# Kernel tuning notes

Measured on AMD Instinct MI355X. Metric: run time of the kernel, lower is better.

The kernel has to match this reference:

```python
import jax, jax.numpy as jnp
import numpy as np

NUM_CLASSES = 21
EPS = 1e-6


def setup_inputs() -> dict:
    key = jax.random.key(0)
    k1, k2, k3 = jax.random.split(key, 3)
    feats = jax.random.normal(k1, (8, 256, 64, 64), dtype=jnp.float32)
    preds = jax.random.normal(k2, (8, NUM_CLASSES, 256, 256), dtype=jnp.float32)
    # labels in [0, 22): includes nclass=21 which acts as an ignore label
    masks = jax.random.randint(k3, (8, 256, 256), 0, 22, dtype=jnp.int64)
    return {"feats": feats, "preds": preds, "masks": masks}


def reference(feats, preds, masks):
    B, C = feats.shape[0], feats.shape[1]
    H, W = masks.shape[-2:]
    K = NUM_CLASSES

    # argmax over class logits -> predicted label map [B, H, W]
    pred_lbl = jnp.argmax(preds, axis=1)

    # bilinear upsample (align_corners=False, matches half-pixel resize)
    feats_up = jax.image.resize(feats, (B, C, H, W), method="bilinear")

    cls = jnp.arange(K)
    # one-hot of gt mask and of predictions; labels >= K (incl. 255) fall in
    # the dropped last channel of one_hot_2d, i.e. match no class here.
    gt_oh = (masks[:, None, :, :] == cls[None, :, None, None])      # [B,K,H,W]
    pr_oh = (pred_lbl[:, None, :, :] == cls[None, :, None, None])   # [B,K,H,W]
    joint = (gt_oh & pr_oh).astype(feats_up.dtype)                  # [B,K,H,W]

    counts = joint.sum(axis=(2, 3))                                  # [B,K]
    sums = jnp.einsum("bchw,bkhw->bkc", feats_up, joint)            # [B,K,C]

    # per-image class means (absent classes -> 0/eps = 0), then batch mean
    proto = (sums / (counts[..., None] + EPS)).mean(axis=0)          # [K,C]
    return proto
```

## Files before the change

kernel.cpp:

```cpp
#include <hip/hip_runtime.h>

#define KC   21
#define BB   8
#define CC   256
#define HWP  65536
#define SRC  4096
#define NS   128
#define PC   32
#define FST  257

#define WSF_PARTW 32768
#define WSF_PART  (WSF_PARTW + BB*NS*KC)

__global__ __launch_bounds__(256, 2)
void k1_classify(const float* __restrict__ preds,
                 const int*   __restrict__ masks,
                 unsigned char* __restrict__ L,
                 float* __restrict__ out)
{
    int tid = threadIdx.x;
    if (blockIdx.x == 0) {
        float4* o4 = reinterpret_cast<float4*>(out);
#pragma unroll
        for (int i = 0; i < (KC * CC / 4 + 255) / 256; ++i) {
            int j = tid + i * 256;
            if (j < KC * CC / 4) o4[j] = make_float4(0.f, 0.f, 0.f, 0.f);
        }
    }

    int idx = blockIdx.x * 256 + tid;
    int b   = idx >> 14;
    int hw4 = (idx & 16383) << 2;

    const float* pb = preds + (size_t)b * KC * HWP + hw4;
    float va[4][KC];
#pragma unroll
    for (int k = 0; k < KC; ++k) {
        float4 t = *reinterpret_cast<const float4*>(pb + (size_t)k * HWP);
        va[0][k] = t.x; va[1][k] = t.y; va[2][k] = t.z; va[3][k] = t.w;
    }

    int4 mm = *reinterpret_cast<const int4*>(masks + b * HWP + hw4);
    int mk[4] = { mm.x, mm.y, mm.z, mm.w };

    uchar4 r;
    unsigned char* rp = reinterpret_cast<unsigned char*>(&r);
#pragma unroll
    for (int j = 0; j < 4; ++j) {
        float best = va[j][0];
        int   bi   = 0;
#pragma unroll
        for (int k = 1; k < KC; ++k) {
            if (va[j][k] > best) { best = va[j][k]; bi = k; }
        }
        rp[j] = (mk[j] == bi) ? (unsigned char)bi : (unsigned char)255;
    }
    *reinterpret_cast<uchar4*>(L + (size_t)b * HWP + hw4) = r;
}

__global__ __launch_bounds__(256, 4)
void k2_contract(const float* __restrict__ feats,
                 const unsigned char* __restrict__ L,
                 float* __restrict__ partial,
                 float* __restrict__ partialw)
{
    __shared__ float fs[PC * FST];
    __shared__ float ws[KC * PC];
    int s = blockIdx.x, b = blockIdx.y;
    int tid = threadIdx.x;
    int y = s >> 1, x0c = (s & 1) * PC;
    int p0 = y * 64 + x0c;

    if (tid < KC * PC / 4)
        *reinterpret_cast<float4*>(ws + tid * 4) = make_float4(0.f, 0.f, 0.f, 0.f);
    __syncthreads();

    {
        int q = tid & 7, c0 = tid >> 3;
#pragma unroll
        for (int i = 0; i < 8; ++i) {
            int c = i * 32 + c0;
            float4 f4 = *reinterpret_cast<const float4*>(
                feats + (size_t)(b * CC + c) * SRC + p0 + q * 4);
            fs[(q * 4 + 0) * FST + c] = f4.x;
            fs[(q * 4 + 1) * FST + c] = f4.y;
            fs[(q * 4 + 2) * FST + c] = f4.z;
            fs[(q * 4 + 3) * FST + c] = f4.w;
        }
    }

    {
        int r = tid >> 5, cb = tid & 31;
        int h = 4 * y - 2 + r;
        if ((unsigned)h < 256u) {
            float sy = h * 0.25f - 0.375f;
            int   yt = (int)floorf(sy);
            float wy = sy - (float)yt;
            int ya = yt < 0 ? 0 : yt;
            int yb = yt + 1 > 63 ? 63 : yt + 1;
            float wyy = ((ya == y) ? (1.f - wy) : 0.f) + ((yb == y) ? wy : 0.f);
            if (wyy != 0.f) {
                const unsigned char* Lrow = L + ((size_t)b << 16) + ((size_t)h << 8);
                int wb0 = 4 * x0c - 2;
#pragma unroll
                for (int j = 0; j < 5; ++j) {
                    int col = cb + j * 32;
                    int w = wb0 + col;
                    if (col < 136 && (unsigned)w < 256u) {
                        int k = Lrow[w];
                        if (k < KC) {
                            float sx = w * 0.25f - 0.375f;
                            int   xt = (int)floorf(sx);
                            float wx = sx - (float)xt;
                            int xa = xt < 0 ? 0 : xt;
                            int xb = xt + 1 > 63 ? 63 : xt + 1;
                            if (xa >= x0c && xa < x0c + PC)
                                atomicAdd(&ws[k * PC + xa - x0c], wyy * (1.f - wx));
                            if (xb >= x0c && xb < x0c + PC)
                                atomicAdd(&ws[k * PC + xb - x0c], wyy * wx);
                        }
                    }
                }
            }
        }
    }
    __syncthreads();

    int cp   = tid & 127;
    int psub = tid >> 7;
    int pw   = psub * 16;

    float f0[16], f1[16];
#pragma unroll
    for (int p = 0; p < 16; ++p) {
        f0[p] = fs[(pw + p) * FST + cp];
        f1[p] = fs[(pw + p) * FST + cp + 128];
    }

    float swcnt = 0.f;
    if (tid < KC) {
#pragma unroll
        for (int p = 0; p < PC; ++p) swcnt += ws[tid * PC + ((p + tid) & (PC - 1))];
    }
    __syncthreads();

    float acc0[KC], acc1[KC];
#pragma unroll
    for (int k = 0; k < KC; ++k) {
        const float* wk = ws + k * PC + pw;
        float a00 = 0.f, a01 = 0.f, a02 = 0.f, a03 = 0.f;
        float a10 = 0.f, a11 = 0.f, a12 = 0.f, a13 = 0.f;
#pragma unroll
        for (int q = 0; q < 4; ++q) {
            float4 w4 = *reinterpret_cast<const float4*>(wk + q * 4);
            a00 += w4.x * f0[q * 4 + 0];
            a01 += w4.y * f0[q * 4 + 1];
            a02 += w4.z * f0[q * 4 + 2];
            a03 += w4.w * f0[q * 4 + 3];
            a10 += w4.x * f1[q * 4 + 0];
            a11 += w4.y * f1[q * 4 + 1];
            a12 += w4.z * f1[q * 4 + 2];
            a13 += w4.w * f1[q * 4 + 3];
        }
        acc0[k] = (a00 + a01) + (a02 + a03);
        acc1[k] = (a10 + a11) + (a12 + a13);
    }

    float* scr = fs;
    if (psub == 1) {
#pragma unroll
        for (int k = 0; k < KC; ++k) {
            scr[k * 256 + cp]       = acc0[k];
            scr[k * 256 + 128 + cp] = acc1[k];
        }
    }
    __syncthreads();
    if (psub == 0) {
        float* op = partial + ((size_t)(b * NS + s)) * KC * CC + cp;
#pragma unroll
        for (int k = 0; k < KC; ++k) {
            op[(size_t)k * CC]       = acc0[k] + scr[k * 256 + cp];
            op[(size_t)k * CC + 128] = acc1[k] + scr[k * 256 + 128 + cp];
        }
    }

    if (tid < KC)
        partialw[(size_t)(b * NS + s) * KC + tid] = swcnt;
}

__global__ __launch_bounds__(256)
void k3_finalize(const float* __restrict__ partial,
                 const float* __restrict__ partialw,
                 float* __restrict__ out)
{
    int k = blockIdx.x, b = blockIdx.y;
    int tid = threadIdx.x;

    const float* base = partial + ((size_t)(b * NS) * KC + k) * CC + tid;
    float acc = 0.f;
#pragma unroll 8
    for (int s = 0; s < NS; ++s) acc += base[(size_t)s * KC * CC];

    __shared__ float red[2];
    float v = 0.f;
    if (tid < NS) v = partialw[(size_t)(b * NS + tid) * KC + k];
#pragma unroll
    for (int off = 32; off; off >>= 1) v += __shfl_down(v, off);
    if (tid < NS && (tid & 63) == 0) red[tid >> 6] = v;
    __syncthreads();
    float cnt = red[0] + red[1];

    atomicAdd(&out[k * CC + tid], acc / (8.f * (cnt + 1e-6f)));
}

extern "C" void kernel_launch(void* const* d_in, const int* in_sizes, int n_in,
                              void* d_out, int out_size, void* d_ws, size_t ws_size,
                              hipStream_t stream) {
    const float* feats = (const float*)d_in[0];
    const float* preds = (const float*)d_in[1];
    const int*   masks = (const int*)  d_in[2];
    float* out = (float*)d_out;

    float* wsf = (float*)d_ws;
    unsigned char* L = (unsigned char*)d_ws;
    float* partialw = wsf + WSF_PARTW;
    float* partial  = wsf + WSF_PART;

    k1_classify<<<(BB * HWP / 4) / 256, 256, 0, stream>>>(preds, masks, L, out);
    k2_contract<<<dim3(NS, BB), 256, 0, stream>>>(feats, L, partial, partialw);
    k3_finalize<<<dim3(KC, BB), 256, 0, stream>>>(partial, partialw, out);
}
```

Measured before the change: 37.14 us.

## Load features straight to registers with 512-thread blocks in the contraction kernel

The contraction kernel now uses 512 threads per block, one thread per channel and 16-pixel half. Each thread reads its 16 feature values directly from global memory into registers, so the transposing shared-memory staging buffer and one barrier are gone. Shared memory shrinks to the weight table plus a reduction scratch area, which should allow more resident blocks. The partial-count workspace offset also moves past the full label buffer, which removes an overlap with it. The trade-off is less coalesced global reads, since neighbouring threads now read different channel rows.

```diff
diff --git a/kernel.cpp b/kernel.cpp
--- a/kernel.cpp
+++ b/kernel.cpp
@@ -7,9 +7,8 @@
 #define SRC  4096
 #define NS   128
 #define PC   32
-#define FST  257
-
-#define WSF_PARTW 32768
+
+#define WSF_PARTW 131072
 #define WSF_PART  (WSF_PARTW + BB*NS*KC)
 
 __global__ __launch_bounds__(256, 2)
@@ -58,39 +57,40 @@
     *reinterpret_cast<uchar4*>(L + (size_t)b * HWP + hw4) = r;
 }
 
-__global__ __launch_bounds__(256, 4)
+__global__ __launch_bounds__(512, 8)
 void k2_contract(const float* __restrict__ feats,
                  const unsigned char* __restrict__ L,
                  float* __restrict__ partial,
                  float* __restrict__ partialw)
 {
-    __shared__ float fs[PC * FST];
     __shared__ float ws[KC * PC];
+    __shared__ float scr[KC * CC];
     int s = blockIdx.x, b = blockIdx.y;
     int tid = threadIdx.x;
     int y = s >> 1, x0c = (s & 1) * PC;
     int p0 = y * 64 + x0c;
 
+    int cp   = tid & 255;
+    int psub = tid >> 8;
+    int pw   = psub * 16;
+
     if (tid < KC * PC / 4)
         *reinterpret_cast<float4*>(ws + tid * 4) = make_float4(0.f, 0.f, 0.f, 0.f);
-    __syncthreads();
-
+
+    float f[16];
     {
-        int q = tid & 7, c0 = tid >> 3;
-#pragma unroll
-        for (int i = 0; i < 8; ++i) {
-            int c = i * 32 + c0;
-            float4 f4 = *reinterpret_cast<const float4*>(
-                feats + (size_t)(b * CC + c) * SRC + p0 + q * 4);
-            fs[(q * 4 + 0) * FST + c] = f4.x;
-            fs[(q * 4 + 1) * FST + c] = f4.y;
-            fs[(q * 4 + 2) * FST + c] = f4.z;
-            fs[(q * 4 + 3) * FST + c] = f4.w;
-        }
-    }
+        const float* frow = feats + (size_t)(b * CC + cp) * SRC + p0 + pw;
+#pragma unroll
+        for (int q = 0; q < 4; ++q) {
+            float4 t = *reinterpret_cast<const float4*>(frow + q * 4);
+            f[q * 4 + 0] = t.x; f[q * 4 + 1] = t.y;
+            f[q * 4 + 2] = t.z; f[q * 4 + 3] = t.w;
+        }
+    }
+    __syncthreads();
 
     {
-        int r = tid >> 5, cb = tid & 31;
+        int r = tid >> 6, cb = tid & 63;
         int h = 4 * y - 2 + r;
         if ((unsigned)h < 256u) {
             float sy = h * 0.25f - 0.375f;
@@ -103,8 +103,8 @@
                 const unsigned char* Lrow = L + ((size_t)b << 16) + ((size_t)h << 8);
                 int wb0 = 4 * x0c - 2;
 #pragma unroll
-                for (int j = 0; j < 5; ++j) {
-                    int col = cb + j * 32;
+                for (int j = 0; j < 3; ++j) {
+                    int col = cb + j * 64;
                     int w = wb0 + col;
                     if (col < 136 && (unsigned)w < 256u) {
                         int k = Lrow[w];
@@ -126,62 +126,38 @@
     }
     __syncthreads();
 
-    int cp   = tid & 127;
-    int psub = tid >> 7;
-    int pw   = psub * 16;
-
-    float f0[16], f1[16];
-#pragma unroll
-    for (int p = 0; p < 16; ++p) {
-        f0[p] = fs[(pw + p) * FST + cp];
-        f1[p] = fs[(pw + p) * FST + cp + 128];
-    }
-
     float swcnt = 0.f;
     if (tid < KC) {
 #pragma unroll
         for (int p = 0; p < PC; ++p) swcnt += ws[tid * PC + ((p + tid) & (PC - 1))];
     }
-    __syncthreads();
-
-    float acc0[KC], acc1[KC];
+
+    float acc[KC];
 #pragma unroll
     for (int k = 0; k < KC; ++k) {
         const float* wk = ws + k * PC + pw;
-        float a00 = 0.f, a01 = 0.f, a02 = 0.f, a03 = 0.f;
-        float a10 = 0.f, a11 = 0.f, a12 = 0.f, a13 = 0.f;
+        float a0 = 0.f, a1 = 0.f, a2 = 0.f, a3 = 0.f;
 #pragma unroll
         for (int q = 0; q < 4; ++q) {
             float4 w4 = *reinterpret_cast<const float4*>(wk + q * 4);
-            a00 += w4.x * f0[q * 4 + 0];
-            a01 += w4.y * f0[q * 4 + 1];
-            a02 += w4.z * f0[q * 4 + 2];
-            a03 += w4.w * f0[q * 4 + 3];
-            a10 += w4.x * f1[q * 4 + 0];
-            a11 += w4.y * f1[q * 4 + 1];
-            a12 += w4.z * f1[q * 4 + 2];
-            a13 += w4.w * f1[q * 4 + 3];
-        }
-        acc0[k] = (a00 + a01) + (a02 + a03);
-        acc1[k] = (a10 + a11) + (a12 + a13);
-    }
-
-    float* scr = fs;
+            a0 += w4.x * f[q * 4 + 0];
+            a1 += w4.y * f[q * 4 + 1];
+            a2 += w4.z * f[q * 4 + 2];
+            a3 += w4.w * f[q * 4 + 3];
+        }
+        acc[k] = (a0 + a1) + (a2 + a3);
+    }
+
     if (psub == 1) {
 #pragma unroll
-        for (int k = 0; k < KC; ++k) {
-            scr[k * 256 + cp]       = acc0[k];
-            scr[k * 256 + 128 + cp] = acc1[k];
-        }
+        for (int k = 0; k < KC; ++k) scr[k * CC + cp] = acc[k];
     }
     __syncthreads();
     if (psub == 0) {
         float* op = partial + ((size_t)(b * NS + s)) * KC * CC + cp;
 #pragma unroll
-        for (int k = 0; k < KC; ++k) {
-            op[(size_t)k * CC]       = acc0[k] + scr[k * 256 + cp];
-            op[(size_t)k * CC + 128] = acc1[k] + scr[k * 256 + 128 + cp];
-        }
+        for (int k = 0; k < KC; ++k)
+            op[(size_t)k * CC] = acc[k] + scr[k * CC + cp];
     }
 
     if (tid < KC)
@@ -227,6 +203,6 @@
     float* partial  = wsf + WSF_PART;
 
     k1_classify<<<(BB * HWP / 4) / 256, 256, 0, stream>>>(preds, masks, L, out);
-    k2_contract<<<dim3(NS, BB), 256, 0, stream>>>(feats, L, partial, partialw);
+    k2_contract<<<dim3(NS, BB), 512, 0, stream>>>(feats, L, partial, partialw);
     k3_finalize<<<dim3(KC, BB), 256, 0, stream>>>(partial, partialw, out);
 }
```

Result: no change. 36.67 us (-1.3%).
